# Kernel tuning notes

Hardware: AMD Instinct MI355X
Metric: run time of the kernel (lower is better)

Reference implementation:

```python
import jax, jax.numpy as jnp
import numpy as np

B, S, D = 2, 2048, 1024
H, HD = 16, 64

def setup_inputs() -> dict:
    key = jax.random.key(0)
    k1, k2, k3 = jax.random.split(key, 3)
    x = jax.random.normal(k1, (B, S, D), dtype=jnp.float32)
    w_qkv = jax.random.normal(k2, (3 * D, D), dtype=jnp.float32) * (D ** -0.5)
    w_out = jax.random.normal(k3, (D, D), dtype=jnp.float32) * (D ** -0.5)
    return {"x": x, "w_qkv": w_qkv, "w_out": w_out}

def reference(x, w_qkv, w_out):
    scale = HD ** -0.5
    # qkv projection: torch Linear applies x @ W.T
    qkv = jnp.einsum('bsd,ed->bse', x, w_qkv)            # [B,S,3D]
    qkv = qkv.reshape(B, S, 3, H, HD)
    q, k, v = qkv[:, :, 0], qkv[:, :, 1], qkv[:, :, 2]   # [B,S,H,HD]
    # scores: explicit matmul-softmax-matmul (unfused, as in source)
    scores = jnp.einsum('bqhd,bkhd->bhqk', q, k) * scale  # [B,H,S,S]
    attn = jax.nn.softmax(scores, axis=-1)
    out = jnp.einsum('bhqk,bkhd->bqhd', attn, v)          # [B,S,H,HD]
    out = out.reshape(B, S, D)
    return jnp.einsum('bsd,ed->bse', out, w_out)
```

## Files before the change

kernel.cpp:

```cpp
#include <hip/hip_runtime.h>
#include <hip/hip_bf16.h>
#include <math.h>

#define B_ 2
#define S_ 2048
#define D_ 1024
#define H_ 16
#define HD_ 64

typedef short bf16x8 __attribute__((ext_vector_type(8)));
typedef short bf16x4 __attribute__((ext_vector_type(4)));
typedef float f32x4 __attribute__((ext_vector_type(4)));

#define MFMA32(a, b, c) __builtin_amdgcn_mfma_f32_16x16x32_bf16(a, b, c, 0, 0, 0)
#define MFMA16(a, b, c) __builtin_amdgcn_mfma_f32_16x16x16bf16_1k(a, b, c, 0, 0, 0)

static __device__ __forceinline__ unsigned short f2bf(float f) {
    union { float f; unsigned u; } v = {f};
    return (unsigned short)((v.u + 0x7fffu + ((v.u >> 16) & 1u)) >> 16);
}

static __device__ __forceinline__ unsigned pk2bf(float a, float b) {
    __hip_bfloat162 h = __float22bfloat162_rn(make_float2(a, b));
    unsigned r;
    __builtin_memcpy(&r, &h, 4);
    return r;
}

static __device__ __forceinline__ void gl2lds16(const void* g, void* l) {
    __builtin_amdgcn_global_load_lds((const __attribute__((address_space(1))) unsigned int*)g,
                                     (__attribute__((address_space(3))) unsigned int*)l,
                                     16, 0, 0);
}

static __device__ __forceinline__ bf16x8 scaleQ(bf16x8 v, float s) {
    union { bf16x8 v; unsigned u[4]; } a, r;
    a.v = v;
    #pragma unroll
    for (int i = 0; i < 4; ++i) {
        float lo = __uint_as_float(a.u[i] << 16);
        float hi = __uint_as_float(a.u[i] & 0xffff0000u);
        r.u[i] = pk2bf(lo * s, hi * s);
    }
    return r.v;
}

__global__ __launch_bounds__(256) void cvt_all(const float* __restrict__ x,
                                               const float* __restrict__ wq,
                                               const float* __restrict__ wo,
                                               unsigned short* __restrict__ xb,
                                               unsigned short* __restrict__ wqb,
                                               unsigned short* __restrict__ wob) {
    const int N0 = 1048576, N1 = 786432, N2 = 262144;
    int stride = gridDim.x * blockDim.x;
    for (int i = blockIdx.x * blockDim.x + threadIdx.x; i < N0 + N1 + N2; i += stride) {
        const float4* src; ushort4* dst; int j;
        if (i < N0)            { src = (const float4*)x;  dst = (ushort4*)xb;  j = i; }
        else if (i < N0 + N1)  { src = (const float4*)wq; dst = (ushort4*)wqb; j = i - N0; }
        else                   { src = (const float4*)wo; dst = (ushort4*)wob; j = i - N0 - N1; }
        float4 v = src[j];
        ushort4 o;
        o.x = f2bf(v.x); o.y = f2bf(v.y); o.z = f2bf(v.z); o.w = f2bf(v.w);
        dst[j] = o;
    }
}

template <int BN>
__global__ __launch_bounds__(256) void gemm_nt_b(const unsigned short* __restrict__ A,
                                                 const unsigned short* __restrict__ Bm,
                                                 void* __restrict__ Cout,
                                                 int M, int N, int K, int c_bf16) {
    constexpr int BM = 128, BK = 32;
    constexpr int MI = (BN == 128) ? 4 : 2;
    constexpr int NI = 4;
    constexpr int SEGS = (BM + BN) / 16;
    __shared__ unsigned short As[BM * BK];
    __shared__ unsigned short Bs[BN * BK];

    const int tid = threadIdx.x;
    const int wave = tid >> 6, lane = tid & 63;
    const int m16 = lane & 15, quad = lane >> 4;
    const int wrow = (BN == 128) ? (wave >> 1) * 64 : wave * 32;
    const int wcol = (BN == 128) ? (wave & 1) * 64 : 0;
    const int row0 = blockIdx.y * BM, col0 = blockIdx.x * BN;

    const int lrow = lane >> 2;
    const int lk = (lane & 3) * 8;

    f32x4 acc[MI][NI] = {};

    for (int k0 = 0; k0 < K; k0 += BK) {
        __syncthreads();
        for (int s = wave; s < SEGS; s += 4) {
            if (s < BM / 16) {
                gl2lds16(&A[(size_t)(row0 + s * 16 + lrow) * K + k0 + lk],
                         &As[s * 16 * BK]);
            } else {
                int t = s - BM / 16;
                gl2lds16(&Bm[(size_t)(col0 + t * 16 + lrow) * K + k0 + lk],
                         &Bs[t * 16 * BK]);
            }
        }
        __asm__ volatile("s_waitcnt vmcnt(0)" ::: "memory");
        __syncthreads();

        bf16x8 af[MI], bfr[NI];
        #pragma unroll
        for (int mi = 0; mi < MI; ++mi)
            af[mi] = *(const bf16x8*)&As[(wrow + mi * 16 + m16) * BK + quad * 8];
        #pragma unroll
        for (int ni = 0; ni < NI; ++ni)
            bfr[ni] = *(const bf16x8*)&Bs[(wcol + ni * 16 + m16) * BK + quad * 8];
        #pragma unroll
        for (int mi = 0; mi < MI; ++mi)
            #pragma unroll
            for (int ni = 0; ni < NI; ++ni)
                acc[mi][ni] = MFMA32(af[mi], bfr[ni], acc[mi][ni]);
    }

    #pragma unroll
    for (int mi = 0; mi < MI; ++mi) {
        #pragma unroll
        for (int r = 0; r < 4; ++r) {
            size_t grow = row0 + wrow + mi * 16 + quad * 4 + r;
            #pragma unroll
            for (int ni = 0; ni < NI; ++ni) {
                size_t gcol = col0 + wcol + ni * 16 + m16;
                if (c_bf16)
                    ((unsigned short*)Cout)[grow * N + gcol] = f2bf(acc[mi][ni][r]);
                else
                    ((float*)Cout)[grow * N + gcol] = acc[mi][ni][r];
            }
        }
    }
}

__global__ __launch_bounds__(256) void transpose_v(const unsigned short* __restrict__ qkv,
                                                   unsigned short* __restrict__ vt) {
    __shared__ unsigned short T[64 * 72];
    const int bid = blockIdx.x;
    const int bh = bid & 31, st = bid >> 5;
    const int b = bh >> 4, h = bh & 15;
    const int tid = threadIdx.x;

    #pragma unroll
    for (int i = 0; i < 2; ++i) {
        int idx = tid + i * 256;
        int r = idx >> 3, c8 = (idx & 7) * 8;
        *(uint4*)&T[r * 72 + c8] =
            *(const uint4*)(qkv + (size_t)(b * S_ + st * 64 + r) * (3 * D_) + 2 * D_ + h * HD_ + c8);
    }
    __syncthreads();
    #pragma unroll
    for (int i = 0; i < 2; ++i) {
        int idx = tid + i * 256;
        int d = idx >> 3, s8 = (idx & 7) * 8;
        unsigned short a[8];
        #pragma unroll
        for (int j = 0; j < 8; ++j) a[j] = T[(s8 + j) * 72 + d];
        *(uint4*)(vt + ((size_t)bh * 64 + d) * S_ + st * 64 + s8) = *(uint4*)a;
    }
}

__global__ __launch_bounds__(256) void attn_mfma(const unsigned short* __restrict__ qkv,
                                                 const unsigned short* __restrict__ vt,
                                                 unsigned short* __restrict__ out) {
    __shared__ unsigned short Ks[2][128 * 64];
    __shared__ unsigned short Vs[2][128 * 64];

    const int id = blockIdx.x;
    const int bh = ((id >> 3) & 3) * 8 + (id & 7);
    const int b = bh >> 4, h = bh & 15;
    const int q0 = (id >> 5) * 128;

    const int tid = threadIdx.x;
    const int wave = tid >> 6, lane = tid & 63;
    const int m16 = lane & 15, quad = lane >> 4;

    const float QS = 0.125f * 1.44269504089f;

    bf16x8 qf0[2], qf1[2];
    #pragma unroll
    for (int g = 0; g < 2; ++g) {
        const unsigned short* qrow =
            qkv + ((size_t)b * S_ + q0 + wave * 32 + g * 16 + m16) * (3 * D_) + h * HD_;
        qf0[g] = scaleQ(*(const bf16x8*)(qrow + quad * 8), QS);
        qf1[g] = scaleQ(*(const bf16x8*)(qrow + 32 + quad * 8), QS);
    }

    f32x4 o[2][4] = {};
    f32x4 ol[2] = {};
    const bf16x4 onesf = {(short)0x3F80, (short)0x3F80, (short)0x3F80, (short)0x3F80};

    const unsigned short* kbase = qkv + (size_t)b * S_ * 3 * D_ + D_ + h * HD_;
    const unsigned short* vtbase = vt + (size_t)bh * 64 * S_;

    const int lr8 = lane >> 3;
    const int lsrc = (lane & 7) ^ lr8;

    int vaddr[4][4];
    #pragma unroll
    for (int dt = 0; dt < 4; ++dt) {
        int d = dt * 16 + m16;
        #pragma unroll
        for (int nt = 0; nt < 4; ++nt) {
            int kc = nt * 2 + (quad >> 1);
            vaddr[dt][nt] = d * 64 + ((kc ^ (m16 & 7)) * 8) + (quad & 1) * 4;
        }
    }

    auto issueDMA = [&](int t, int buf) {
        const unsigned short* kt = kbase + (size_t)t * 128 * (3 * D_);
        const unsigned short* vtt = vtbase + t * 128;
        #pragma unroll
        for (int i = 0; i < 4; ++i) {
            int gi = wave * 4 + i;
            int r = gi * 8 + lr8;
            gl2lds16(kt + (size_t)r * (3 * D_) + lsrc * 8, &Ks[buf][gi * 512]);
            int panel = gi >> 3, vd = (gi & 7) * 8 + lr8;
            gl2lds16(vtt + (size_t)vd * S_ + panel * 64 + lsrc * 8, &Vs[buf][gi * 512]);
        }
    };

    issueDMA(0, 0);
    __asm__ volatile("s_waitcnt vmcnt(0)" ::: "memory");
    __syncthreads();
    issueDMA(1, 1);

    for (int t = 0; t < S_ / 128; ++t) {
        const int buf = t & 1;

        #pragma unroll
        for (int h2 = 0; h2 < 2; ++h2) {
            const unsigned short* Kp = &Ks[buf][h2 * 4096];
            const unsigned short* Vp = &Vs[buf][h2 * 4096];

            bf16x4 pf[2][4];
            #pragma unroll
            for (int nt = 0; nt < 4; ++nt) {
                int a0 = (nt * 16 + m16) * 64 + ((quad ^ (m16 & 7)) * 8);
                bf16x8 kf0 = *(const bf16x8*)&Kp[a0];
                bf16x8 kf1 = *(const bf16x8*)&Kp[a0 ^ 32];
                #pragma unroll
                for (int g = 0; g < 2; ++g) {
                    f32x4 z = {0.f, 0.f, 0.f, 0.f};
                    z = MFMA32(kf0, qf0[g], z);
                    z = MFMA32(kf1, qf1[g], z);
                    float p0 = __builtin_amdgcn_exp2f(z[0]);
                    float p1 = __builtin_amdgcn_exp2f(z[1]);
                    float p2 = __builtin_amdgcn_exp2f(z[2]);
                    float p3 = __builtin_amdgcn_exp2f(z[3]);
                    union { unsigned u[2]; bf16x4 v; } pk;
                    pk.u[0] = pk2bf(p0, p1);
                    pk.u[1] = pk2bf(p2, p3);
                    pf[g][nt] = pk.v;
                    ol[g] = MFMA16(pf[g][nt], onesf, ol[g]);
                }
            }

            #pragma unroll
            for (int nt = 0; nt < 4; ++nt)
                #pragma unroll
                for (int dt = 0; dt < 4; ++dt) {
                    bf16x4 vf = *(const bf16x4*)&Vp[vaddr[dt][nt]];
                    o[0][dt] = MFMA16(pf[0][nt], vf, o[0][dt]);
                    o[1][dt] = MFMA16(pf[1][nt], vf, o[1][dt]);
                }
        }

        __asm__ volatile("s_waitcnt vmcnt(0)" ::: "memory");
        __syncthreads();
        if (t + 2 < S_ / 128) issueDMA(t + 2, buf);
    }

    #pragma unroll
    for (int g = 0; g < 2; ++g)
        #pragma unroll
        for (int r = 0; r < 4; ++r) {
            float inv = 1.f / ol[g][r];
            size_t row = (size_t)b * S_ + q0 + wave * 32 + g * 16 + quad * 4 + r;
            unsigned short* op = out + row * D_ + h * HD_;
            #pragma unroll
            for (int dt = 0; dt < 4; ++dt)
                op[dt * 16 + m16] = f2bf(o[g][dt][r] * inv);
        }
}

extern "C" void kernel_launch(void* const* d_in, const int* in_sizes, int n_in,
                              void* d_out, int out_size, void* d_ws, size_t ws_size,
                              hipStream_t stream) {
    const float* x     = (const float*)d_in[0];
    const float* w_qkv = (const float*)d_in[1];
    const float* w_out = (const float*)d_in[2];
    float* out = (float*)d_out;

    const size_t n_x = (size_t)B_ * S_ * D_;
    const size_t n_wqkv = (size_t)3 * D_ * D_;
    const size_t n_wout = (size_t)D_ * D_;

    unsigned short* xb    = (unsigned short*)d_ws;
    unsigned short* wqkvb = xb + n_x;
    unsigned short* woutb = wqkvb + n_wqkv;
    unsigned short* qkvb  = woutb + n_wout;
    unsigned short* attnb = qkvb + (size_t)B_ * S_ * 3 * D_;
    unsigned short* vtb   = attnb + n_x;

    dim3 blk(256);

    cvt_all<<<2048, blk, 0, stream>>>(x, w_qkv, w_out, xb, wqkvb, woutb);

    gemm_nt_b<128><<<dim3(3 * D_ / 128, B_ * S_ / 128), blk, 0, stream>>>(
        xb, wqkvb, qkvb, B_ * S_, 3 * D_, D_, 1);

    transpose_v<<<1024, blk, 0, stream>>>(qkvb, vtb);

    attn_mfma<<<512, blk, 0, stream>>>(qkvb, vtb, attnb);

    gemm_nt_b<64><<<dim3(D_ / 64, B_ * S_ / 128), blk, 0, stream>>>(
        attnb, woutb, out, B_ * S_, D_, D_, 0);
}
```

Before: 205.2 us.

## Split attention block across 8 waves with 16 query rows each

The attention kernel now launches 512 threads (8 waves) per block, and each wave handles 16 query rows instead of 32. The same 128-query tile is covered, K/V DMA loading is spread over 8 waves, and per-wave register state is halved. The aim is more waves in flight to hide latency, at the cost of each K/V fragment read from LDS being reused by only one query group instead of two, which doubles LDS read traffic per MFMA.

```diff
diff --git a/kernel.cpp b/kernel.cpp
--- a/kernel.cpp
+++ b/kernel.cpp
@@ -162,9 +162,9 @@
     }
 }
 
-__global__ __launch_bounds__(256) void attn_mfma(const unsigned short* __restrict__ qkv,
-                                                 const unsigned short* __restrict__ vt,
-                                                 unsigned short* __restrict__ out) {
+__global__ __launch_bounds__(512, 4) void attn_mfma(const unsigned short* __restrict__ qkv,
+                                                    const unsigned short* __restrict__ vt,
+                                                    unsigned short* __restrict__ out) {
     __shared__ unsigned short Ks[2][128 * 64];
     __shared__ unsigned short Vs[2][128 * 64];
 
@@ -179,17 +179,16 @@
 
     const float QS = 0.125f * 1.44269504089f;
 
-    bf16x8 qf0[2], qf1[2];
-    #pragma unroll
-    for (int g = 0; g < 2; ++g) {
+    bf16x8 qf0, qf1;
+    {
         const unsigned short* qrow =
-            qkv + ((size_t)b * S_ + q0 + wave * 32 + g * 16 + m16) * (3 * D_) + h * HD_;
-        qf0[g] = scaleQ(*(const bf16x8*)(qrow + quad * 8), QS);
-        qf1[g] = scaleQ(*(const bf16x8*)(qrow + 32 + quad * 8), QS);
-    }
-
-    f32x4 o[2][4] = {};
-    f32x4 ol[2] = {};
+            qkv + ((size_t)b * S_ + q0 + wave * 16 + m16) * (3 * D_) + h * HD_;
+        qf0 = scaleQ(*(const bf16x8*)(qrow + quad * 8), QS);
+        qf1 = scaleQ(*(const bf16x8*)(qrow + 32 + quad * 8), QS);
+    }
+
+    f32x4 o[4] = {};
+    f32x4 ol = {};
     const bf16x4 onesf = {(short)0x3F80, (short)0x3F80, (short)0x3F80, (short)0x3F80};
 
     const unsigned short* kbase = qkv + (size_t)b * S_ * 3 * D_ + D_ + h * HD_;
@@ -213,8 +212,8 @@
         const unsigned short* kt = kbase + (size_t)t * 128 * (3 * D_);
         const unsigned short* vtt = vtbase + t * 128;
         #pragma unroll
-        for (int i = 0; i < 4; ++i) {
-            int gi = wave * 4 + i;
+        for (int i = 0; i < 2; ++i) {
+            int gi = wave * 2 + i;
             int r = gi * 8 + lr8;
             gl2lds16(kt + (size_t)r * (3 * D_) + lsrc * 8, &Ks[buf][gi * 512]);
             int panel = gi >> 3, vd = (gi & 7) * 8 + lr8;
@@ -235,27 +234,24 @@
             const unsigned short* Kp = &Ks[buf][h2 * 4096];
             const unsigned short* Vp = &Vs[buf][h2 * 4096];
 
-            bf16x4 pf[2][4];
+            bf16x4 pf[4];
             #pragma unroll
             for (int nt = 0; nt < 4; ++nt) {
                 int a0 = (nt * 16 + m16) * 64 + ((quad ^ (m16 & 7)) * 8);
                 bf16x8 kf0 = *(const bf16x8*)&Kp[a0];
                 bf16x8 kf1 = *(const bf16x8*)&Kp[a0 ^ 32];
-                #pragma unroll
-                for (int g = 0; g < 2; ++g) {
-                    f32x4 z = {0.f, 0.f, 0.f, 0.f};
-                    z = MFMA32(kf0, qf0[g], z);
-                    z = MFMA32(kf1, qf1[g], z);
-                    float p0 = __builtin_amdgcn_exp2f(z[0]);
-                    float p1 = __builtin_amdgcn_exp2f(z[1]);
-                    float p2 = __builtin_amdgcn_exp2f(z[2]);
-                    float p3 = __builtin_amdgcn_exp2f(z[3]);
-                    union { unsigned u[2]; bf16x4 v; } pk;
-                    pk.u[0] = pk2bf(p0, p1);
-                    pk.u[1] = pk2bf(p2, p3);
-                    pf[g][nt] = pk.v;
-                    ol[g] = MFMA16(pf[g][nt], onesf, ol[g]);
-                }
+                f32x4 z = {0.f, 0.f, 0.f, 0.f};
+                z = MFMA32(kf0, qf0, z);
+                z = MFMA32(kf1, qf1, z);
+                float p0 = __builtin_amdgcn_exp2f(z[0]);
+                float p1 = __builtin_amdgcn_exp2f(z[1]);
+                float p2 = __builtin_amdgcn_exp2f(z[2]);
+                float p3 = __builtin_amdgcn_exp2f(z[3]);
+                union { unsigned u[2]; bf16x4 v; } pk;
+                pk.u[0] = pk2bf(p0, p1);
+                pk.u[1] = pk2bf(p2, p3);
+                pf[nt] = pk.v;
+                ol = MFMA16(pf[nt], onesf, ol);
             }
 
             #pragma unroll
@@ -263,8 +259,7 @@
                 #pragma unroll
                 for (int dt = 0; dt < 4; ++dt) {
                     bf16x4 vf = *(const bf16x4*)&Vp[vaddr[dt][nt]];
-                    o[0][dt] = MFMA16(pf[0][nt], vf, o[0][dt]);
-                    o[1][dt] = MFMA16(pf[1][nt], vf, o[1][dt]);
+                    o[dt] = MFMA16(pf[nt], vf, o[dt]);
                 }
         }
 
@@ -274,16 +269,14 @@
     }
 
     #pragma unroll
-    for (int g = 0; g < 2; ++g)
-        #pragma unroll
-        for (int r = 0; r < 4; ++r) {
-            float inv = 1.f / ol[g][r];
-            size_t row = (size_t)b * S_ + q0 + wave * 32 + g * 16 + quad * 4 + r;
-            unsigned short* op = out + row * D_ + h * HD_;
-            #pragma unroll
-            for (int dt = 0; dt < 4; ++dt)
-                op[dt * 16 + m16] = f2bf(o[g][dt][r] * inv);
-        }
+    for (int r = 0; r < 4; ++r) {
+        float inv = 1.f / ol[r];
+        size_t row = (size_t)b * S_ + q0 + wave * 16 + quad * 4 + r;
+        unsigned short* op = out + row * D_ + h * HD_;
+        #pragma unroll
+        for (int dt = 0; dt < 4; ++dt)
+            op[dt * 16 + m16] = f2bf(o[dt][r] * inv);
+    }
 }
 
 extern "C" void kernel_launch(void* const* d_in, const int* in_sizes, int n_in,
@@ -314,7 +307,7 @@
 
     transpose_v<<<1024, blk, 0, stream>>>(qkvb, vtb);
 
-    attn_mfma<<<512, blk, 0, stream>>>(qkvb, vtb, attnb);
+    attn_mfma<<<512, dim3(512), 0, stream>>>(qkvb, vtb, attnb);
 
     gemm_nt_b<64><<<dim3(D_ / 64, B_ * S_ / 128), blk, 0, stream>>>(
         attnb, woutb, out, B_ * S_, D_, D_, 0);
```

Measured after the change: 202.6 us. Within noise of the previous version (-1.3%).

## Split attention KV sequence across two wave groups per block with LDS reduction

Applied to the files above, without the earlier changes.

The attention kernel now launches 512 threads per block. The 8 waves form two groups, and each group handles alternating 64-key tiles of the same 128 query rows, so the key dimension is split inside the block. Partial outputs and row sums are merged through LDS at the end before normalisation. This is meant to double the waves available to hide MFMA, exp and LDS latency within a block, at the cost of an extra reduction step and different LDS and register pressure under launch_bounds(512,4).

```diff
diff --git a/kernel.cpp b/kernel.cpp
--- a/kernel.cpp
+++ b/kernel.cpp
@@ -162,11 +162,10 @@
     }
 }
 
-__global__ __launch_bounds__(256) void attn_mfma(const unsigned short* __restrict__ qkv,
-                                                 const unsigned short* __restrict__ vt,
-                                                 unsigned short* __restrict__ out) {
-    __shared__ unsigned short Ks[2][128 * 64];
-    __shared__ unsigned short Vs[2][128 * 64];
+__global__ __launch_bounds__(512, 4) void attn_mfma(const unsigned short* __restrict__ qkv,
+                                                    const unsigned short* __restrict__ vt,
+                                                    unsigned short* __restrict__ out) {
+    __shared__ unsigned short L[2][16384];
 
     const int id = blockIdx.x;
     const int bh = ((id >> 3) & 3) * 8 + (id & 7);
@@ -175,6 +174,8 @@
 
     const int tid = threadIdx.x;
     const int wave = tid >> 6, lane = tid & 63;
+    const int grp = wave >> 2;
+    const int qw = wave & 3;
     const int m16 = lane & 15, quad = lane >> 4;
 
     const float QS = 0.125f * 1.44269504089f;
@@ -183,7 +184,7 @@
     #pragma unroll
     for (int g = 0; g < 2; ++g) {
         const unsigned short* qrow =
-            qkv + ((size_t)b * S_ + q0 + wave * 32 + g * 16 + m16) * (3 * D_) + h * HD_;
+            qkv + ((size_t)b * S_ + q0 + qw * 32 + g * 16 + m16) * (3 * D_) + h * HD_;
         qf0[g] = scaleQ(*(const bf16x8*)(qrow + quad * 8), QS);
         qf1[g] = scaleQ(*(const bf16x8*)(qrow + 32 + quad * 8), QS);
     }
@@ -198,27 +199,35 @@
     const int lr8 = lane >> 3;
     const int lsrc = (lane & 7) ^ lr8;
 
-    int vaddr[4][4];
-    #pragma unroll
-    for (int dt = 0; dt < 4; ++dt) {
-        int d = dt * 16 + m16;
-        #pragma unroll
-        for (int nt = 0; nt < 4; ++nt) {
-            int kc = nt * 2 + (quad >> 1);
-            vaddr[dt][nt] = d * 64 + ((kc ^ (m16 & 7)) * 8) + (quad & 1) * 4;
-        }
-    }
-
-    auto issueDMA = [&](int t, int buf) {
-        const unsigned short* kt = kbase + (size_t)t * 128 * (3 * D_);
-        const unsigned short* vtt = vtbase + t * 128;
-        #pragma unroll
-        for (int i = 0; i < 4; ++i) {
-            int gi = wave * 4 + i;
-            int r = gi * 8 + lr8;
-            gl2lds16(kt + (size_t)r * (3 * D_) + lsrc * 8, &Ks[buf][gi * 512]);
-            int panel = gi >> 3, vd = (gi & 7) * 8 + lr8;
-            gl2lds16(vtt + (size_t)vd * S_ + panel * 64 + lsrc * 8, &Vs[buf][gi * 512]);
+    const int kaddr0 = m16 * 64 + ((quad ^ (m16 & 7)) * 8);
+    const int kaddr1 = kaddr0 ^ 32;
+    int va[4];
+    #pragma unroll
+    for (int nt = 0; nt < 4; ++nt) {
+        int kc = nt * 2 + (quad >> 1);
+        va[nt] = m16 * 64 + ((kc ^ (m16 & 7)) * 8) + (quad & 1) * 4;
+    }
+
+    auto issueDMA = [&](int pair, int buf) {
+        const int mat = wave >> 1;
+        const int tt = pair * 2 + (mat >> 1);
+        unsigned short* dstb = &L[buf][mat * 4096];
+        if ((mat & 1) == 0) {
+            const unsigned short* kt = kbase + (size_t)tt * 64 * (3 * D_);
+            #pragma unroll
+            for (int i = 0; i < 4; ++i) {
+                int gi = (wave & 1) * 4 + i;
+                gl2lds16(kt + (size_t)(gi * 8 + lr8) * (3 * D_) + lsrc * 8,
+                         dstb + gi * 512);
+            }
+        } else {
+            const unsigned short* vtt = vtbase + tt * 64;
+            #pragma unroll
+            for (int i = 0; i < 4; ++i) {
+                int gi = (wave & 1) * 4 + i;
+                gl2lds16(vtt + (size_t)(gi * 8 + lr8) * S_ + lsrc * 8,
+                         dstb + gi * 512);
+            }
         }
     };
 
@@ -227,63 +236,79 @@
     __syncthreads();
     issueDMA(1, 1);
 
-    for (int t = 0; t < S_ / 128; ++t) {
-        const int buf = t & 1;
-
-        #pragma unroll
-        for (int h2 = 0; h2 < 2; ++h2) {
-            const unsigned short* Kp = &Ks[buf][h2 * 4096];
-            const unsigned short* Vp = &Vs[buf][h2 * 4096];
-
-            bf16x4 pf[2][4];
-            #pragma unroll
-            for (int nt = 0; nt < 4; ++nt) {
-                int a0 = (nt * 16 + m16) * 64 + ((quad ^ (m16 & 7)) * 8);
-                bf16x8 kf0 = *(const bf16x8*)&Kp[a0];
-                bf16x8 kf1 = *(const bf16x8*)&Kp[a0 ^ 32];
-                #pragma unroll
-                for (int g = 0; g < 2; ++g) {
-                    f32x4 z = {0.f, 0.f, 0.f, 0.f};
-                    z = MFMA32(kf0, qf0[g], z);
-                    z = MFMA32(kf1, qf1[g], z);
-                    float p0 = __builtin_amdgcn_exp2f(z[0]);
-                    float p1 = __builtin_amdgcn_exp2f(z[1]);
-                    float p2 = __builtin_amdgcn_exp2f(z[2]);
-                    float p3 = __builtin_amdgcn_exp2f(z[3]);
-                    union { unsigned u[2]; bf16x4 v; } pk;
-                    pk.u[0] = pk2bf(p0, p1);
-                    pk.u[1] = pk2bf(p2, p3);
-                    pf[g][nt] = pk.v;
-                    ol[g] = MFMA16(pf[g][nt], onesf, ol[g]);
-                }
-            }
-
-            #pragma unroll
-            for (int nt = 0; nt < 4; ++nt)
-                #pragma unroll
-                for (int dt = 0; dt < 4; ++dt) {
-                    bf16x4 vf = *(const bf16x4*)&Vp[vaddr[dt][nt]];
-                    o[0][dt] = MFMA16(pf[0][nt], vf, o[0][dt]);
-                    o[1][dt] = MFMA16(pf[1][nt], vf, o[1][dt]);
-                }
-        }
+    for (int s = 0; s < 16; ++s) {
+        const int buf = s & 1;
+        const unsigned short* Kp = &L[buf][grp * 8192];
+        const unsigned short* Vp = Kp + 4096;
+
+        bf16x4 pf[2][4];
+        #pragma unroll
+        for (int nt = 0; nt < 4; ++nt) {
+            bf16x8 kf0 = *(const bf16x8*)&Kp[kaddr0 + nt * 1024];
+            bf16x8 kf1 = *(const bf16x8*)&Kp[kaddr1 + nt * 1024];
+            #pragma unroll
+            for (int g = 0; g < 2; ++g) {
+                f32x4 z = {0.f, 0.f, 0.f, 0.f};
+                z = MFMA32(kf0, qf0[g], z);
+                z = MFMA32(kf1, qf1[g], z);
+                float p0 = __builtin_amdgcn_exp2f(z[0]);
+                float p1 = __builtin_amdgcn_exp2f(z[1]);
+                float p2 = __builtin_amdgcn_exp2f(z[2]);
+                float p3 = __builtin_amdgcn_exp2f(z[3]);
+                union { unsigned u[2]; bf16x4 v; } pk;
+                pk.u[0] = pk2bf(p0, p1);
+                pk.u[1] = pk2bf(p2, p3);
+                pf[g][nt] = pk.v;
+                ol[g] = MFMA16(pf[g][nt], onesf, ol[g]);
+            }
+        }
+
+        #pragma unroll
+        for (int nt = 0; nt < 4; ++nt)
+            #pragma unroll
+            for (int dt = 0; dt < 4; ++dt) {
+                bf16x4 vf = *(const bf16x4*)&Vp[va[nt] + dt * 1024];
+                o[0][dt] = MFMA16(pf[0][nt], vf, o[0][dt]);
+                o[1][dt] = MFMA16(pf[1][nt], vf, o[1][dt]);
+            }
 
         __asm__ volatile("s_waitcnt vmcnt(0)" ::: "memory");
         __syncthreads();
-        if (t + 2 < S_ / 128) issueDMA(t + 2, buf);
-    }
-
-    #pragma unroll
-    for (int g = 0; g < 2; ++g)
-        #pragma unroll
-        for (int r = 0; r < 4; ++r) {
-            float inv = 1.f / ol[g][r];
-            size_t row = (size_t)b * S_ + q0 + wave * 32 + g * 16 + quad * 4 + r;
-            unsigned short* op = out + row * D_ + h * HD_;
+        if (s + 2 < 16) issueDMA(s + 2, buf);
+    }
+
+    float* M = (float*)&L[0][0];
+    const int mb = (qw * 64 + lane) * 44;
+    if (grp == 1) {
+        #pragma unroll
+        for (int g = 0; g < 2; ++g) {
             #pragma unroll
             for (int dt = 0; dt < 4; ++dt)
-                op[dt * 16 + m16] = f2bf(o[g][dt][r] * inv);
-        }
+                *(f32x4*)&M[mb + (g * 4 + dt) * 4] = o[g][dt];
+            *(f32x4*)&M[mb + 32 + g * 4] = ol[g];
+        }
+    }
+    __syncthreads();
+    if (grp == 0) {
+        #pragma unroll
+        for (int g = 0; g < 2; ++g) {
+            #pragma unroll
+            for (int dt = 0; dt < 4; ++dt)
+                o[g][dt] += *(const f32x4*)&M[mb + (g * 4 + dt) * 4];
+            ol[g] += *(const f32x4*)&M[mb + 32 + g * 4];
+        }
+        #pragma unroll
+        for (int g = 0; g < 2; ++g)
+            #pragma unroll
+            for (int r = 0; r < 4; ++r) {
+                float inv = 1.f / ol[g][r];
+                size_t row = (size_t)b * S_ + q0 + qw * 32 + g * 16 + quad * 4 + r;
+                unsigned short* op = out + row * D_ + h * HD_;
+                #pragma unroll
+                for (int dt = 0; dt < 4; ++dt)
+                    op[dt * 16 + m16] = f2bf(o[g][dt][r] * inv);
+            }
+    }
 }
 
 extern "C" void kernel_launch(void* const* d_in, const int* in_sizes, int n_in,
@@ -314,7 +339,7 @@
 
     transpose_v<<<1024, blk, 0, stream>>>(qkvb, vtb);
 
-    attn_mfma<<<512, blk, 0, stream>>>(qkvb, vtb, attnb);
+    attn_mfma<<<512, dim3(512), 0, stream>>>(qkvb, vtb, attnb);
 
     gemm_nt_b<64><<<dim3(D_ / 64, B_ * S_ / 128), blk, 0, stream>>>(
         attnb, woutb, out, B_ * S_, D_, D_, 0);
```

New measurement: 197.9 us. 1.04x faster.

## Split attention key range across wave groups with LDS reduction, doubling grid

Applied to the files above, without the earlier changes.

The attention kernel now launches 1024 blocks of 512 threads, each covering 64 query rows instead of 128. Inside a block, four wave groups each handle a different 16-key slice of every 64-key tile. Their partial output and row-sum accumulators are reduced through shared memory at the end. The goal is more parallelism and occupancy on the attention stage, since the original grid had only 512 blocks. The price is a serialized three-phase LDS reduction, half as many keys per tile per iteration, and a raised MFMA priority around the PV loop.

```diff
diff --git a/kernel.cpp b/kernel.cpp
--- a/kernel.cpp
+++ b/kernel.cpp
@@ -162,19 +162,20 @@
     }
 }
 
-__global__ __launch_bounds__(256) void attn_mfma(const unsigned short* __restrict__ qkv,
-                                                 const unsigned short* __restrict__ vt,
-                                                 unsigned short* __restrict__ out) {
-    __shared__ unsigned short Ks[2][128 * 64];
-    __shared__ unsigned short Vs[2][128 * 64];
+__global__ __launch_bounds__(512, 6) void attn_mfma(const unsigned short* __restrict__ qkv,
+                                                    const unsigned short* __restrict__ vt,
+                                                    unsigned short* __restrict__ out) {
+    __shared__ unsigned short L[2][8192];
 
     const int id = blockIdx.x;
     const int bh = ((id >> 3) & 3) * 8 + (id & 7);
     const int b = bh >> 4, h = bh & 15;
-    const int q0 = (id >> 5) * 128;
+    const int q0 = (id >> 5) * 64;
 
     const int tid = threadIdx.x;
     const int wave = tid >> 6, lane = tid & 63;
+    const int grp = wave >> 1;
+    const int qw = wave & 1;
     const int m16 = lane & 15, quad = lane >> 4;
 
     const float QS = 0.125f * 1.44269504089f;
@@ -183,7 +184,7 @@
     #pragma unroll
     for (int g = 0; g < 2; ++g) {
         const unsigned short* qrow =
-            qkv + ((size_t)b * S_ + q0 + wave * 32 + g * 16 + m16) * (3 * D_) + h * HD_;
+            qkv + ((size_t)b * S_ + q0 + qw * 32 + g * 16 + m16) * (3 * D_) + h * HD_;
         qf0[g] = scaleQ(*(const bf16x8*)(qrow + quad * 8), QS);
         qf1[g] = scaleQ(*(const bf16x8*)(qrow + 32 + quad * 8), QS);
     }
@@ -198,27 +199,23 @@
     const int lr8 = lane >> 3;
     const int lsrc = (lane & 7) ^ lr8;
 
-    int vaddr[4][4];
-    #pragma unroll
-    for (int dt = 0; dt < 4; ++dt) {
-        int d = dt * 16 + m16;
-        #pragma unroll
-        for (int nt = 0; nt < 4; ++nt) {
-            int kc = nt * 2 + (quad >> 1);
-            vaddr[dt][nt] = d * 64 + ((kc ^ (m16 & 7)) * 8) + (quad & 1) * 4;
-        }
-    }
+    const int kaddr0 = m16 * 64 + ((quad ^ (m16 & 7)) * 8);
+    const int kaddr1 = kaddr0 ^ 32;
+    const int kc = grp * 2 + (quad >> 1);
+    const int va = m16 * 64 + ((kc ^ (m16 & 7)) * 8) + (quad & 1) * 4;
 
     auto issueDMA = [&](int t, int buf) {
-        const unsigned short* kt = kbase + (size_t)t * 128 * (3 * D_);
-        const unsigned short* vtt = vtbase + t * 128;
-        #pragma unroll
-        for (int i = 0; i < 4; ++i) {
-            int gi = wave * 4 + i;
-            int r = gi * 8 + lr8;
-            gl2lds16(kt + (size_t)r * (3 * D_) + lsrc * 8, &Ks[buf][gi * 512]);
-            int panel = gi >> 3, vd = (gi & 7) * 8 + lr8;
-            gl2lds16(vtt + (size_t)vd * S_ + panel * 64 + lsrc * 8, &Vs[buf][gi * 512]);
+        #pragma unroll
+        for (int i = 0; i < 2; ++i) {
+            int gi = wave * 2 + i;
+            if (gi < 8) {
+                gl2lds16(kbase + (size_t)(t * 64 + gi * 8 + lr8) * (3 * D_) + lsrc * 8,
+                         &L[buf][gi * 512]);
+            } else {
+                int j = gi - 8;
+                gl2lds16(vtbase + (size_t)(j * 8 + lr8) * S_ + t * 64 + lsrc * 8,
+                         &L[buf][4096 + j * 512]);
+            }
         }
     };
 
@@ -227,63 +224,83 @@
     __syncthreads();
     issueDMA(1, 1);
 
-    for (int t = 0; t < S_ / 128; ++t) {
+    for (int t = 0; t < 32; ++t) {
         const int buf = t & 1;
-
-        #pragma unroll
-        for (int h2 = 0; h2 < 2; ++h2) {
-            const unsigned short* Kp = &Ks[buf][h2 * 4096];
-            const unsigned short* Vp = &Vs[buf][h2 * 4096];
-
-            bf16x4 pf[2][4];
-            #pragma unroll
-            for (int nt = 0; nt < 4; ++nt) {
-                int a0 = (nt * 16 + m16) * 64 + ((quad ^ (m16 & 7)) * 8);
-                bf16x8 kf0 = *(const bf16x8*)&Kp[a0];
-                bf16x8 kf1 = *(const bf16x8*)&Kp[a0 ^ 32];
+        const unsigned short* Kp = &L[buf][grp * 1024];
+        const unsigned short* Vp = &L[buf][4096];
+
+        bf16x8 kf0 = *(const bf16x8*)&Kp[kaddr0];
+        bf16x8 kf1 = *(const bf16x8*)&Kp[kaddr1];
+        bf16x4 pf[2];
+        #pragma unroll
+        for (int g = 0; g < 2; ++g) {
+            f32x4 z = {0.f, 0.f, 0.f, 0.f};
+            z = MFMA32(kf0, qf0[g], z);
+            z = MFMA32(kf1, qf1[g], z);
+            float p0 = __builtin_amdgcn_exp2f(z[0]);
+            float p1 = __builtin_amdgcn_exp2f(z[1]);
+            float p2 = __builtin_amdgcn_exp2f(z[2]);
+            float p3 = __builtin_amdgcn_exp2f(z[3]);
+            union { unsigned u[2]; bf16x4 v; } pk;
+            pk.u[0] = pk2bf(p0, p1);
+            pk.u[1] = pk2bf(p2, p3);
+            pf[g] = pk.v;
+            ol[g] = MFMA16(pf[g], onesf, ol[g]);
+        }
+
+        __builtin_amdgcn_s_setprio(1);
+        #pragma unroll
+        for (int dt = 0; dt < 4; ++dt) {
+            bf16x4 vf = *(const bf16x4*)&Vp[va + dt * 1024];
+            o[0][dt] = MFMA16(pf[0], vf, o[0][dt]);
+            o[1][dt] = MFMA16(pf[1], vf, o[1][dt]);
+        }
+        __builtin_amdgcn_s_setprio(0);
+
+        __asm__ volatile("s_waitcnt vmcnt(0)" ::: "memory");
+        __syncthreads();
+        if (t + 2 < 32) issueDMA(t + 2, buf);
+    }
+
+    float* Mg = (float*)&L[0][0];
+    const int mb = (qw * 64 + lane) * 40;
+    #pragma unroll 1
+    for (int ph = 1; ph < 4; ++ph) {
+        if (grp == ph) {
+            #pragma unroll
+            for (int g = 0; g < 2; ++g) {
                 #pragma unroll
-                for (int g = 0; g < 2; ++g) {
-                    f32x4 z = {0.f, 0.f, 0.f, 0.f};
-                    z = MFMA32(kf0, qf0[g], z);
-                    z = MFMA32(kf1, qf1[g], z);
-                    float p0 = __builtin_amdgcn_exp2f(z[0]);
-                    float p1 = __builtin_amdgcn_exp2f(z[1]);
-                    float p2 = __builtin_amdgcn_exp2f(z[2]);
-                    float p3 = __builtin_amdgcn_exp2f(z[3]);
-                    union { unsigned u[2]; bf16x4 v; } pk;
-                    pk.u[0] = pk2bf(p0, p1);
-                    pk.u[1] = pk2bf(p2, p3);
-                    pf[g][nt] = pk.v;
-                    ol[g] = MFMA16(pf[g][nt], onesf, ol[g]);
-                }
-            }
-
-            #pragma unroll
-            for (int nt = 0; nt < 4; ++nt)
+                for (int dt = 0; dt < 4; ++dt)
+                    *(f32x4*)&Mg[mb + (g * 4 + dt) * 4] = o[g][dt];
+                *(f32x4*)&Mg[mb + 32 + g * 4] = ol[g];
+            }
+        }
+        __syncthreads();
+        if (grp == 0) {
+            #pragma unroll
+            for (int g = 0; g < 2; ++g) {
                 #pragma unroll
-                for (int dt = 0; dt < 4; ++dt) {
-                    bf16x4 vf = *(const bf16x4*)&Vp[vaddr[dt][nt]];
-                    o[0][dt] = MFMA16(pf[0][nt], vf, o[0][dt]);
-                    o[1][dt] = MFMA16(pf[1][nt], vf, o[1][dt]);
-                }
-        }
-
-        __asm__ volatile("s_waitcnt vmcnt(0)" ::: "memory");
-        __syncthreads();
-        if (t + 2 < S_ / 128) issueDMA(t + 2, buf);
-    }
-
-    #pragma unroll
-    for (int g = 0; g < 2; ++g)
-        #pragma unroll
-        for (int r = 0; r < 4; ++r) {
-            float inv = 1.f / ol[g][r];
-            size_t row = (size_t)b * S_ + q0 + wave * 32 + g * 16 + quad * 4 + r;
-            unsigned short* op = out + row * D_ + h * HD_;
-            #pragma unroll
-            for (int dt = 0; dt < 4; ++dt)
-                op[dt * 16 + m16] = f2bf(o[g][dt][r] * inv);
-        }
+                for (int dt = 0; dt < 4; ++dt)
+                    o[g][dt] += *(const f32x4*)&Mg[mb + (g * 4 + dt) * 4];
+                ol[g] += *(const f32x4*)&Mg[mb + 32 + g * 4];
+            }
+        }
+        __syncthreads();
+    }
+
+    if (grp == 0) {
+        #pragma unroll
+        for (int g = 0; g < 2; ++g)
+            #pragma unroll
+            for (int r = 0; r < 4; ++r) {
+                float inv = 1.f / ol[g][r];
+                size_t row = (size_t)b * S_ + q0 + qw * 32 + g * 16 + quad * 4 + r;
+                unsigned short* op = out + row * D_ + h * HD_;
+                #pragma unroll
+                for (int dt = 0; dt < 4; ++dt)
+                    op[dt * 16 + m16] = f2bf(o[g][dt][r] * inv);
+            }
+    }
 }
 
 extern "C" void kernel_launch(void* const* d_in, const int* in_sizes, int n_in,
@@ -314,7 +331,7 @@
 
     transpose_v<<<1024, blk, 0, stream>>>(qkvb, vtb);
 
-    attn_mfma<<<512, blk, 0, stream>>>(qkvb, vtb, attnb);
+    attn_mfma<<<1024, dim3(512), 0, stream>>>(qkvb, vtb, attnb);
 
     gemm_nt_b<64><<<dim3(D_ / 64, B_ * S_ / 128), blk, 0, stream>>>(
         attnb, woutb, out, B_ * S_, D_, D_, 0);
```

After: 264.6 us. 1.29x slower.
